# Kernel tuning notes

Hardware: AMD Instinct MI355X
Metric: run time of the kernel (lower is better)

Reference implementation:

```python
import jax, jax.numpy as jnp
import numpy as np

NUM_GROUPS = 4
EPS = 1e-6


def group_norm(x, gamma, beta):
    # x: [B, C, H, W, L]
    b, ch = x.shape[0], x.shape[1]
    xr = x.reshape(b, NUM_GROUPS, ch // NUM_GROUPS, -1)
    mean = xr.mean(axis=(2, 3), keepdims=True)
    var = xr.var(axis=(2, 3), keepdims=True)
    xn = ((xr - mean) * jax.lax.rsqrt(var + EPS)).reshape(x.shape)
    return xn * gamma.reshape(1, ch, 1, 1, 1) + beta.reshape(1, ch, 1, 1, 1)


def conv1(x, w, bias):
    # 1x1x1 Conv3d == channel-mixing linear: w [Cout, Cin]
    return jnp.einsum('bchwl,oc->bohwl', x, w) + bias.reshape(1, -1, 1, 1, 1)


def setup_inputs() -> dict:
    key = jax.random.key(0)
    ks = jax.random.split(key, 16)
    C = 128
    shp = (2, C, 16, 16, 16)
    scale = 1.0 / np.sqrt(C)
    inp = {
        'x': jax.random.normal(ks[0], shp, dtype=jnp.float32),
        'c': jax.random.normal(ks[1], shp, dtype=jnp.float32),
        'g1': jnp.ones((C,), jnp.float32),
        'b1': jnp.zeros((C,), jnp.float32),
        'g2': jnp.ones((C,), jnp.float32),
        'b2': jnp.zeros((C,), jnp.float32),
        'wq': jax.random.normal(ks[2], (C, C), jnp.float32) * scale,
        'bq': jnp.zeros((C,), jnp.float32),
        'wk': jax.random.normal(ks[3], (C, C), jnp.float32) * scale,
        'bk': jnp.zeros((C,), jnp.float32),
        'wv': jax.random.normal(ks[4], (C, C), jnp.float32) * scale,
        'bv': jnp.zeros((C,), jnp.float32),
        'wp': jax.random.normal(ks[5], (C, C), jnp.float32) * scale,
        'bp': jnp.zeros((C,), jnp.float32),
    }
    return inp


def reference(x, c, g1, b1, g2, b2, wq, bq, wk, bk, wv, bv, wp, bp):
    h_ = group_norm(x, g1, b1)   # norm_1(x)
    c_ = group_norm(c, g2, b2)   # norm_2(c)
    q = conv1(c_, wq, bq)        # query from conditioning c
    k = conv1(h_, wk, bk)
    v = conv1(h_, wv, bv)
    b, ch, h, w, l = q.shape
    n = h * w * l
    qf = q.reshape(b, ch, n)
    kf = k.reshape(b, ch, n)
    vf = v.reshape(b, ch, n)
    # scores[b, i, j] = <q[:, i], k[:, j]> * C^-0.5
    scores = jnp.einsum('bci,bcj->bij', qf, kf) * (ch ** -0.5)
    attn = jax.nn.softmax(scores, axis=2)
    # out[b, c, i] = sum_j v[b, c, j] * attn[b, i, j]
    out = jnp.einsum('bcj,bij->bci', vf, attn).reshape(b, ch, h, w, l)
    out = conv1(out, wp, bp)
    return x + out
```

## Files before the change

kernel.cpp:

```cpp
#include <hip/hip_runtime.h>
#include <math.h>

#define C 128
#define N 4096
#define B 2
#define CPG 32

typedef __attribute__((ext_vector_type(8))) short bf16x8;
typedef __attribute__((ext_vector_type(4))) float f32x4;

static __device__ __forceinline__ ushort f2bf(float f) {
  unsigned u = __float_as_uint(f);
  unsigned r = (u + 0x7fffu + ((u >> 16) & 1u)) >> 16;
  return (ushort)r;
}

__global__ __launch_bounds__(256) void gn_partial_kernel(
    const float* __restrict__ x, const float* __restrict__ cc,
    const float* __restrict__ wq, const float* __restrict__ wk,
    const float* __restrict__ wv, const float* __restrict__ wp,
    float* __restrict__ stats, ushort* __restrict__ wb) {
  if (blockIdx.y == 2) {
    if (blockIdx.x >= 32) return;
    int idx = (blockIdx.x * 256 + threadIdx.x) * 8;
    const float* srcs[4] = {wq, wk, wv, wp};
    const float* s = srcs[idx >> 14] + (idx & 16383);
    float4 a = *(const float4*)s;
    float4 b2 = *(const float4*)(s + 4);
    ushort h[8];
    h[0] = f2bf(a.x);  h[1] = f2bf(a.y);  h[2] = f2bf(a.z);  h[3] = f2bf(a.w);
    h[4] = f2bf(b2.x); h[5] = f2bf(b2.y); h[6] = f2bf(b2.z); h[7] = f2bf(b2.w);
    *(uint4*)(wb + idx) = *(uint4*)h;
    return;
  }
  const int t = blockIdx.y;
  const int bg = blockIdx.x >> 3, slice = blockIdx.x & 7;
  const float* in = (t == 0) ? x : cc;
  const float4* base = (const float4*)(in + (size_t)bg * CPG * N + slice * 16384);
  float s = 0.f, sq = 0.f;
  #pragma unroll
  for (int k = 0; k < 16; ++k) {
    float4 v = base[threadIdx.x + k * 256];
    s  += v.x + v.y + v.z + v.w;
    sq += v.x * v.x + v.y * v.y + v.z * v.z + v.w * v.w;
  }
  #pragma unroll
  for (int off = 32; off > 0; off >>= 1) {
    s  += __shfl_down(s, off, 64);
    sq += __shfl_down(sq, off, 64);
  }
  __shared__ float ss[4], ssq[4];
  const int wid = threadIdx.x >> 6;
  if ((threadIdx.x & 63) == 0) { ss[wid] = s; ssq[wid] = sq; }
  __syncthreads();
  if (threadIdx.x == 0) {
    atomicAdd(&stats[(t * 8 + bg) * 2 + 0], ss[0] + ss[1] + ss[2] + ss[3]);
    atomicAdd(&stats[(t * 8 + bg) * 2 + 1], ssq[0] + ssq[1] + ssq[2] + ssq[3]);
  }
}

__global__ __launch_bounds__(256) void qkv_kernel(
    const float* __restrict__ x, const float* __restrict__ cc,
    const float* __restrict__ g1, const float* __restrict__ b1,
    const float* __restrict__ g2, const float* __restrict__ b2,
    const ushort* __restrict__ wqb, const ushort* __restrict__ wkb,
    const ushort* __restrict__ wvb,
    const float* __restrict__ bq, const float* __restrict__ bk,
    const float* __restrict__ bv, const float* __restrict__ stats,
    ushort* __restrict__ qt, ushort* __restrict__ kt, ushort* __restrict__ vb) {
  const int zw    = blockIdx.y;
  const int which = zw >> 1;
  const int b     = zw & 1;
  const int i0    = blockIdx.x * 32;
  const int tid   = threadIdx.x;

  const float *in, *bias, *gamma, *beta;
  const ushort* wmat;
  int tensor;
  if (which == 0)      { in = cc; wmat = wqb; bias = bq; gamma = g2; beta = b2; tensor = 1; }
  else if (which == 1) { in = x;  wmat = wkb; bias = bk; gamma = g1; beta = b1; tensor = 0; }
  else                 { in = x;  wmat = wvb; bias = bv; gamma = g1; beta = b1; tensor = 0; }

  __shared__ float a_s[C], d_s[C];
  __shared__ __align__(16) ushort xt[32 * 136];
  if (tid < C) {
    const int ch = tid, g = ch >> 5;
    const float cnt = (float)(CPG * N);
    float S  = stats[(tensor * 8 + b * 4 + g) * 2 + 0];
    float SQ = stats[(tensor * 8 + b * 4 + g) * 2 + 1];
    float mean = S / cnt;
    float var  = SQ / cnt - mean * mean;
    float rstd = rsqrtf(var + 1e-6f);
    float ga = gamma[ch];
    a_s[ch] = rstd * ga;
    d_s[ch] = beta[ch] - mean * rstd * ga;
  }
  __syncthreads();

  {
    const int c = tid >> 1, ih = tid & 1;
    const float* src = in + ((size_t)b * C + c) * N + i0 + ih * 16;
    const float av = a_s[c], dv = d_s[c];
    #pragma unroll
    for (int k4 = 0; k4 < 4; ++k4) {
      float4 v = *(const float4*)(src + k4 * 4);
      const int i = ih * 16 + k4 * 4;
      xt[(i + 0) * 136 + c] = f2bf(fmaf(v.x, av, dv));
      xt[(i + 1) * 136 + c] = f2bf(fmaf(v.y, av, dv));
      xt[(i + 2) * 136 + c] = f2bf(fmaf(v.z, av, dv));
      xt[(i + 3) * 136 + c] = f2bf(fmaf(v.w, av, dv));
    }
  }
  __syncthreads();

  const int w = tid >> 6, lane = tid & 63, quad = lane >> 4, l15 = lane & 15;
  bf16x8 aw[2][4];
  #pragma unroll
  for (int mt2 = 0; mt2 < 2; ++mt2)
    #pragma unroll
    for (int ks = 0; ks < 4; ++ks)
      aw[mt2][ks] = *(const bf16x8*)(wmat + (size_t)(w * 32 + mt2 * 16 + l15) * 128 + ks * 32 + quad * 8);

  f32x4 acc[2][2];
  #pragma unroll
  for (int mt2 = 0; mt2 < 2; ++mt2)
    #pragma unroll
    for (int nt = 0; nt < 2; ++nt) acc[mt2][nt] = (f32x4){0.f, 0.f, 0.f, 0.f};

  #pragma unroll
  for (int nt = 0; nt < 2; ++nt) {
    bf16x8 bo[4];
    #pragma unroll
    for (int ks = 0; ks < 4; ++ks)
      bo[ks] = *(const bf16x8*)(&xt[(nt * 16 + l15) * 136 + ks * 32 + quad * 8]);
    #pragma unroll
    for (int mt2 = 0; mt2 < 2; ++mt2)
      #pragma unroll
      for (int ks = 0; ks < 4; ++ks)
        acc[mt2][nt] = __builtin_amdgcn_mfma_f32_16x16x32_bf16(aw[mt2][ks], bo[ks], acc[mt2][nt], 0, 0, 0);
  }

  #pragma unroll
  for (int mt2 = 0; mt2 < 2; ++mt2) {
    const int ob = w * 32 + mt2 * 16 + quad * 4;
    float4 bb4 = *(const float4*)(bias + ob);
    float bbv[4] = {bb4.x, bb4.y, bb4.z, bb4.w};
    #pragma unroll
    for (int nt = 0; nt < 2; ++nt) {
      const int i = i0 + nt * 16 + l15;
      if (which <= 1) {
        ushort* dst = (which == 0 ? qt : kt);
        ushort h[4];
        #pragma unroll
        for (int r = 0; r < 4; ++r) h[r] = f2bf(acc[mt2][nt][r] + bbv[r]);
        *(uint2*)(dst + ((size_t)b * N + i) * C + ob) = *(uint2*)h;
      } else {
        #pragma unroll
        for (int r = 0; r < 4; ++r)
          vb[((size_t)b * C + ob + r) * N + i] = f2bf(acc[mt2][nt][r] + bbv[r]);
      }
    }
  }
}

__global__ __launch_bounds__(256) void attn_kernel(
    const ushort* __restrict__ qt, const ushort* __restrict__ kt,
    const ushort* __restrict__ vb, float* __restrict__ pml,
    ushort* __restrict__ pO, int part_keys) {
  __shared__ __align__(16) ushort ksts[32 * 136];
  __shared__ __align__(16) ushort vss [128 * 40];
  __shared__ __align__(16) ushort pss [4][16 * 40];

  const int b    = blockIdx.z;
  const int part = blockIdx.y;
  const int i0   = blockIdx.x * 64;
  const int tid  = threadIdx.x;
  const int w    = tid >> 6;
  const int lane = tid & 63;
  const int quad = lane >> 4;
  const int l15  = lane & 15;
  const float scale = 0.08838834764831845f;

  bf16x8 aq[4];
  {
    const ushort* qrow = qt + ((size_t)b * N + i0 + w * 16 + l15) * C;
    #pragma unroll
    for (int ks = 0; ks < 4; ++ks)
      aq[ks] = *(const bf16x8*)(qrow + ks * 32 + quad * 8);
  }

  float lacc[4] = {0.f, 0.f, 0.f, 0.f};
  f32x4 Ofr[8];
  #pragma unroll
  for (int mt = 0; mt < 8; ++mt) Ofr[mt] = (f32x4){0.f, 0.f, 0.f, 0.f};

  const int krow = tid >> 3, kseg = tid & 7;
  const int vc = tid >> 1, vseg = tid & 1;
  const ushort* kbase = kt + ((size_t)b * N + krow) * C + kseg * 16;
  const ushort* vbase = vb + ((size_t)b * C + vc) * N + vseg * 16;
  uint4* dk = (uint4*)(&ksts[krow * 136 + kseg * 16]);
  uint4* dv = (uint4*)(&vss[vc * 40 + vseg * 16]);

  const int tcount = part_keys >> 5;
  const int jbase = part * part_keys;
  uint4 k0, k1, v0, v1;
  {
    const uint4* sk = (const uint4*)(kbase + (size_t)jbase * C);
    k0 = sk[0]; k1 = sk[1];
    const uint4* sv = (const uint4*)(vbase + jbase);
    v0 = sv[0]; v1 = sv[1];
  }

  for (int t = 0; t < tcount; ++t) {
    __syncthreads();
    dk[0] = k0; dk[1] = k1;
    dv[0] = v0; dv[1] = v1;
    __syncthreads();
    if (t + 1 < tcount) {
      const int j1 = jbase + (t + 1) * 32;
      const uint4* sk = (const uint4*)(kbase + (size_t)j1 * C);
      k0 = sk[0]; k1 = sk[1];
      const uint4* sv = (const uint4*)(vbase + j1);
      v0 = sv[0]; v1 = sv[1];
    }

    f32x4 sfr[2];
    #pragma unroll
    for (int nt = 0; nt < 2; ++nt) {
      f32x4 s = (f32x4){0.f, 0.f, 0.f, 0.f};
      #pragma unroll
      for (int ks = 0; ks < 4; ++ks) {
        bf16x8 bk = *(const bf16x8*)(&ksts[(nt * 16 + l15) * 136 + ks * 32 + quad * 8]);
        s = __builtin_amdgcn_mfma_f32_16x16x32_bf16(aq[ks], bk, s, 0, 0, 0);
      }
      sfr[nt] = s;
    }

    #pragma unroll
    for (int r = 0; r < 4; ++r) {
      float p0 = __expf(sfr[0][r] * scale);
      float p1 = __expf(sfr[1][r] * scale);
      pss[w][(quad * 4 + r) * 40 + l15]      = f2bf(p0);
      pss[w][(quad * 4 + r) * 40 + 16 + l15] = f2bf(p1);
      lacc[r] += p0 + p1;
    }
    bf16x8 bpf = *(const bf16x8*)(&pss[w][l15 * 40 + quad * 8]);
    #pragma unroll
    for (int mt = 0; mt < 8; ++mt) {
      bf16x8 av = *(const bf16x8*)(&vss[(mt * 16 + l15) * 40 + quad * 8]);
      Ofr[mt] = __builtin_amdgcn_mfma_f32_16x16x32_bf16(av, bpf, Ofr[mt], 0, 0, 0);
    }
  }

  #pragma unroll
  for (int off = 1; off < 16; off <<= 1)
    #pragma unroll
    for (int r = 0; r < 4; ++r)
      lacc[r] += __shfl_xor(lacc[r], off, 64);

  const size_t blk = ((size_t)part * 64 + blockIdx.x) * 2 + b;
  if (l15 == 0) {
    float* lb = pml + blk * 64;
    #pragma unroll
    for (int r = 0; r < 4; ++r)
      lb[w * 16 + quad * 4 + r] = lacc[r];
  }
  ushort* ob = pO + blk * 8192;
  const int irow = w * 16 + l15;
  #pragma unroll
  for (int mt = 0; mt < 8; ++mt) {
    ushort h[4];
    #pragma unroll
    for (int r = 0; r < 4; ++r) h[r] = f2bf(Ofr[mt][r]);
    *(uint2*)(ob + irow * 128 + mt * 16 + quad * 4) = *(uint2*)h;
  }
}

__global__ __launch_bounds__(256) void combine_kernel(
    const float* __restrict__ x, const float* __restrict__ bp,
    const ushort* __restrict__ wpb, const float* __restrict__ pml,
    const ushort* __restrict__ pO, float* __restrict__ out, int nparts) {
  __shared__ __align__(16) ushort obf[32 * 136];
  __shared__ float linv_s[32];
  const int qt32 = blockIdx.x, b = blockIdx.y;
  const int qt64 = qt32 >> 1, rowoff = (qt32 & 1) * 32;
  const int tid = threadIdx.x;

  if (tid < 32) {
    const int row = rowoff + tid;
    float sum = 0.f;
    for (int p = 0; p < nparts; ++p) {
      const size_t blk = ((size_t)p * 64 + qt64) * 2 + b;
      sum += pml[blk * 64 + row];
    }
    linv_s[tid] = 1.f / sum;
  }
  __syncthreads();

  const int lrow = tid >> 3, seg = tid & 7;
  const int prow = rowoff + lrow;
  float acc[16];
  #pragma unroll
  for (int j = 0; j < 16; ++j) acc[j] = 0.f;
  for (int p = 0; p < nparts; ++p) {
    const size_t blk = ((size_t)p * 64 + qt64) * 2 + b;
    const ushort* src = pO + blk * 8192 + prow * 128 + seg * 16;
    uint4 u[2];
    u[0] = *(const uint4*)src;
    u[1] = *(const uint4*)(src + 8);
    const ushort* hs = (const ushort*)u;
    #pragma unroll
    for (int j = 0; j < 16; ++j)
      acc[j] += __uint_as_float(((unsigned)hs[j]) << 16);
  }
  {
    const float linv = linv_s[lrow];
    ushort h[16];
    #pragma unroll
    for (int j = 0; j < 16; ++j) h[j] = f2bf(acc[j] * linv);
    uint4* d = (uint4*)(&obf[lrow * 136 + seg * 16]);
    d[0] = ((uint4*)h)[0];
    d[1] = ((uint4*)h)[1];
  }
  __syncthreads();

  const int w = tid >> 6, lane = tid & 63, quad = lane >> 4, l15 = lane & 15;
  const int i0 = qt32 * 32;
  bf16x8 awp[2][4];
  #pragma unroll
  for (int mt2 = 0; mt2 < 2; ++mt2)
    #pragma unroll
    for (int ks = 0; ks < 4; ++ks)
      awp[mt2][ks] = *(const bf16x8*)(wpb + (size_t)(w * 32 + mt2 * 16 + l15) * 128 + ks * 32 + quad * 8);

  #pragma unroll
  for (int nt = 0; nt < 2; ++nt) {
    bf16x8 bo[4];
    #pragma unroll
    for (int ks = 0; ks < 4; ++ks)
      bo[ks] = *(const bf16x8*)(&obf[(nt * 16 + l15) * 136 + ks * 32 + quad * 8]);
    #pragma unroll
    for (int mt2 = 0; mt2 < 2; ++mt2) {
      f32x4 acc2 = (f32x4){0.f, 0.f, 0.f, 0.f};
      #pragma unroll
      for (int ks = 0; ks < 4; ++ks)
        acc2 = __builtin_amdgcn_mfma_f32_16x16x32_bf16(awp[mt2][ks], bo[ks], acc2, 0, 0, 0);
      #pragma unroll
      for (int r = 0; r < 4; ++r) {
        const int o = w * 32 + mt2 * 16 + quad * 4 + r;
        const int i = i0 + nt * 16 + l15;
        const size_t off = ((size_t)b * C + o) * (size_t)N + i;
        out[off] = x[off] + acc2[r] + bp[o];
      }
    }
  }
}

extern "C" void kernel_launch(void* const* d_in, const int* in_sizes, int n_in,
                              void* d_out, int out_size, void* d_ws, size_t ws_size,
                              hipStream_t stream) {
  const float* x  = (const float*)d_in[0];
  const float* cc = (const float*)d_in[1];
  const float* g1 = (const float*)d_in[2];
  const float* b1 = (const float*)d_in[3];
  const float* g2 = (const float*)d_in[4];
  const float* b2 = (const float*)d_in[5];
  const float* wq = (const float*)d_in[6];
  const float* bq = (const float*)d_in[7];
  const float* wk = (const float*)d_in[8];
  const float* bk = (const float*)d_in[9];
  const float* wv = (const float*)d_in[10];
  const float* bv = (const float*)d_in[11];
  const float* wp = (const float*)d_in[12];
  const float* bp = (const float*)d_in[13];
  float* out = (float*)d_out;

  const size_t BNC = (size_t)B * N * C;
  char* base = (char*)d_ws;
  float* stats = (float*)base;
  ushort* qt = (ushort*)(base + 4096);
  ushort* kt = qt + BNC;
  ushort* vb = kt + BNC;
  ushort* wb = vb + BNC;
  ushort* wqb = wb, *wkb = wb + 16384, *wvb = wb + 32768, *wpb = wb + 49152;
  float* pml = (float*)(wb + 65536);

  const size_t fixed = 4096 + 3 * BNC * 2 + 131072;
  const size_t per_part = (size_t)64 * 2 * (8192 * 2 + 256);
  const int nparts = (ws_size >= fixed + 8 * per_part) ? 8
                   : (ws_size >= fixed + 4 * per_part) ? 4 : 2;
  ushort* pO = (ushort*)((char*)pml + (size_t)nparts * 32768);
  const int part_keys = N / nparts;

  hipMemsetAsync(stats, 0, 128, stream);
  gn_partial_kernel<<<dim3(64, 3), 256, 0, stream>>>(x, cc, wq, wk, wv, wp, stats, wb);
  qkv_kernel<<<dim3(128, 6), 256, 0, stream>>>(x, cc, g1, b1, g2, b2,
                                               wqb, wkb, wvb, bq, bk, bv, stats,
                                               qt, kt, vb);
  attn_kernel<<<dim3(64, nparts, 2), 256, 0, stream>>>(qt, kt, vb, pml, pO, part_keys);
  combine_kernel<<<dim3(128, 2), 256, 0, stream>>>(x, bp, wpb, pml, pO, out, nparts);
}
```

Measured before the change: 141.2 us.

## Fuse K and V projections per block and drop stats memset via per-slice partials

The QKV kernel now computes K and V together from one normalized x tile, so x is loaded and normalized once instead of twice, with a separate z-slice handling Q from c. Group-norm partial sums are written per slice instead of atomically accumulated, which removes the hipMemsetAsync launch and the atomics. The QKV kernel then sums the 8 slices itself. The workspace per-part size formula is also adjusted. The trade-offs are load imbalance between Q-blocks and KV-blocks, higher register use for the doubled accumulators, and fewer blocks in the grid.

```diff
diff --git a/kernel.cpp b/kernel.cpp
--- a/kernel.cpp
+++ b/kernel.cpp
@@ -54,8 +54,8 @@
   if ((threadIdx.x & 63) == 0) { ss[wid] = s; ssq[wid] = sq; }
   __syncthreads();
   if (threadIdx.x == 0) {
-    atomicAdd(&stats[(t * 8 + bg) * 2 + 0], ss[0] + ss[1] + ss[2] + ss[3]);
-    atomicAdd(&stats[(t * 8 + bg) * 2 + 1], ssq[0] + ssq[1] + ssq[2] + ssq[3]);
+    stats[((t * 8 + bg) * 8 + slice) * 2 + 0] = ss[0] + ss[1] + ss[2] + ss[3];
+    stats[((t * 8 + bg) * 8 + slice) * 2 + 1] = ssq[0] + ssq[1] + ssq[2] + ssq[3];
   }
 }
 
@@ -68,26 +68,28 @@
     const float* __restrict__ bq, const float* __restrict__ bk,
     const float* __restrict__ bv, const float* __restrict__ stats,
     ushort* __restrict__ qt, ushort* __restrict__ kt, ushort* __restrict__ vb) {
-  const int zw    = blockIdx.y;
-  const int which = zw >> 1;
-  const int b     = zw & 1;
+  const int z     = blockIdx.z;
+  const int b     = blockIdx.y;
   const int i0    = blockIdx.x * 32;
   const int tid   = threadIdx.x;
-
-  const float *in, *bias, *gamma, *beta;
-  const ushort* wmat;
-  int tensor;
-  if (which == 0)      { in = cc; wmat = wqb; bias = bq; gamma = g2; beta = b2; tensor = 1; }
-  else if (which == 1) { in = x;  wmat = wkb; bias = bk; gamma = g1; beta = b1; tensor = 0; }
-  else                 { in = x;  wmat = wvb; bias = bv; gamma = g1; beta = b1; tensor = 0; }
+  const int nm    = z ? 2 : 1;
+
+  const float* in    = z ? x : cc;
+  const float* gamma = z ? g1 : g2;
+  const float* beta  = z ? b1 : b2;
+  const int tensor   = z ? 0 : 1;
 
   __shared__ float a_s[C], d_s[C];
   __shared__ __align__(16) ushort xt[32 * 136];
   if (tid < C) {
     const int ch = tid, g = ch >> 5;
     const float cnt = (float)(CPG * N);
-    float S  = stats[(tensor * 8 + b * 4 + g) * 2 + 0];
-    float SQ = stats[(tensor * 8 + b * 4 + g) * 2 + 1];
+    float S = 0.f, SQ = 0.f;
+    #pragma unroll
+    for (int sl = 0; sl < 8; ++sl) {
+      S  += stats[((tensor * 8 + b * 4 + g) * 8 + sl) * 2 + 0];
+      SQ += stats[((tensor * 8 + b * 4 + g) * 8 + sl) * 2 + 1];
+    }
     float mean = S / cnt;
     float var  = SQ / cnt - mean * mean;
     float rstd = rsqrtf(var + 1e-6f);
@@ -114,18 +116,24 @@
   __syncthreads();
 
   const int w = tid >> 6, lane = tid & 63, quad = lane >> 4, l15 = lane & 15;
-  bf16x8 aw[2][4];
-  #pragma unroll
-  for (int mt2 = 0; mt2 < 2; ++mt2)
-    #pragma unroll
-    for (int ks = 0; ks < 4; ++ks)
-      aw[mt2][ks] = *(const bf16x8*)(wmat + (size_t)(w * 32 + mt2 * 16 + l15) * 128 + ks * 32 + quad * 8);
-
-  f32x4 acc[2][2];
-  #pragma unroll
-  for (int mt2 = 0; mt2 < 2; ++mt2)
-    #pragma unroll
-    for (int nt = 0; nt < 2; ++nt) acc[mt2][nt] = (f32x4){0.f, 0.f, 0.f, 0.f};
+  const ushort* wmats[2];
+  wmats[0] = z ? wkb : wqb;
+  wmats[1] = wvb;
+
+  bf16x8 aw[2][2][4];
+  for (int m = 0; m < nm; ++m)
+    #pragma unroll
+    for (int mt2 = 0; mt2 < 2; ++mt2)
+      #pragma unroll
+      for (int ks = 0; ks < 4; ++ks)
+        aw[m][mt2][ks] = *(const bf16x8*)(wmats[m] + (size_t)(w * 32 + mt2 * 16 + l15) * 128 + ks * 32 + quad * 8);
+
+  f32x4 acc[2][2][2];
+  for (int m = 0; m < nm; ++m)
+    #pragma unroll
+    for (int mt2 = 0; mt2 < 2; ++mt2)
+      #pragma unroll
+      for (int nt = 0; nt < 2; ++nt) acc[m][mt2][nt] = (f32x4){0.f, 0.f, 0.f, 0.f};
 
   #pragma unroll
   for (int nt = 0; nt < 2; ++nt) {
@@ -133,31 +141,35 @@
     #pragma unroll
     for (int ks = 0; ks < 4; ++ks)
       bo[ks] = *(const bf16x8*)(&xt[(nt * 16 + l15) * 136 + ks * 32 + quad * 8]);
-    #pragma unroll
-    for (int mt2 = 0; mt2 < 2; ++mt2)
-      #pragma unroll
-      for (int ks = 0; ks < 4; ++ks)
-        acc[mt2][nt] = __builtin_amdgcn_mfma_f32_16x16x32_bf16(aw[mt2][ks], bo[ks], acc[mt2][nt], 0, 0, 0);
-  }
-
-  #pragma unroll
-  for (int mt2 = 0; mt2 < 2; ++mt2) {
-    const int ob = w * 32 + mt2 * 16 + quad * 4;
-    float4 bb4 = *(const float4*)(bias + ob);
-    float bbv[4] = {bb4.x, bb4.y, bb4.z, bb4.w};
-    #pragma unroll
-    for (int nt = 0; nt < 2; ++nt) {
-      const int i = i0 + nt * 16 + l15;
-      if (which <= 1) {
-        ushort* dst = (which == 0 ? qt : kt);
-        ushort h[4];
+    for (int m = 0; m < nm; ++m)
+      #pragma unroll
+      for (int mt2 = 0; mt2 < 2; ++mt2)
         #pragma unroll
-        for (int r = 0; r < 4; ++r) h[r] = f2bf(acc[mt2][nt][r] + bbv[r]);
-        *(uint2*)(dst + ((size_t)b * N + i) * C + ob) = *(uint2*)h;
-      } else {
-        #pragma unroll
-        for (int r = 0; r < 4; ++r)
-          vb[((size_t)b * C + ob + r) * N + i] = f2bf(acc[mt2][nt][r] + bbv[r]);
+        for (int ks = 0; ks < 4; ++ks)
+          acc[m][mt2][nt] = __builtin_amdgcn_mfma_f32_16x16x32_bf16(aw[m][mt2][ks], bo[ks], acc[m][mt2][nt], 0, 0, 0);
+  }
+
+  for (int m = 0; m < nm; ++m) {
+    const float* bias = z ? (m == 0 ? bk : bv) : bq;
+    #pragma unroll
+    for (int mt2 = 0; mt2 < 2; ++mt2) {
+      const int ob = w * 32 + mt2 * 16 + quad * 4;
+      float4 bb4 = *(const float4*)(bias + ob);
+      float bbv[4] = {bb4.x, bb4.y, bb4.z, bb4.w};
+      #pragma unroll
+      for (int nt = 0; nt < 2; ++nt) {
+        const int i = i0 + nt * 16 + l15;
+        if (m == 0) {
+          ushort* dst = z ? kt : qt;
+          ushort h[4];
+          #pragma unroll
+          for (int r = 0; r < 4; ++r) h[r] = f2bf(acc[m][mt2][nt][r] + bbv[r]);
+          *(uint2*)(dst + ((size_t)b * N + i) * C + ob) = *(uint2*)h;
+        } else {
+          #pragma unroll
+          for (int r = 0; r < 4; ++r)
+            vb[((size_t)b * C + ob + r) * N + i] = f2bf(acc[m][mt2][nt][r] + bbv[r]);
+        }
       }
     }
   }
@@ -386,17 +398,16 @@
   float* pml = (float*)(wb + 65536);
 
   const size_t fixed = 4096 + 3 * BNC * 2 + 131072;
-  const size_t per_part = (size_t)64 * 2 * (8192 * 2 + 256);
+  const size_t per_part = 32768 + (size_t)64 * 2 * 8192 * 2;
   const int nparts = (ws_size >= fixed + 8 * per_part) ? 8
                    : (ws_size >= fixed + 4 * per_part) ? 4 : 2;
   ushort* pO = (ushort*)((char*)pml + (size_t)nparts * 32768);
   const int part_keys = N / nparts;
 
-  hipMemsetAsync(stats, 0, 128, stream);
   gn_partial_kernel<<<dim3(64, 3), 256, 0, stream>>>(x, cc, wq, wk, wv, wp, stats, wb);
-  qkv_kernel<<<dim3(128, 6), 256, 0, stream>>>(x, cc, g1, b1, g2, b2,
-                                               wqb, wkb, wvb, bq, bk, bv, stats,
-                                               qt, kt, vb);
+  qkv_kernel<<<dim3(128, 2, 2), 256, 0, stream>>>(x, cc, g1, b1, g2, b2,
+                                                  wqb, wkb, wvb, bq, bk, bv, stats,
+                                                  qt, kt, vb);
   attn_kernel<<<dim3(64, nparts, 2), 256, 0, stream>>>(qt, kt, vb, pml, pO, part_keys);
   combine_kernel<<<dim3(128, 2), 256, 0, stream>>>(x, bp, wpb, pml, pO, out, nparts);
 }
```

New measurement: 151.6 us. 1.07x slower.
